# Kernel optimization log

Hardware: AMD Instinct MI355X
Metric: run time of the kernel (lower is better)

Reference implementation:

```python
import jax, jax.numpy as jnp
import numpy as np

LN_EPS = 1e-5  # torch LayerNorm default


def setup_inputs() -> dict:
    key = jax.random.key(0)
    ks = jax.random.split(key, 6)
    N, E, D = 50000, 800000, 128
    x = jax.random.normal(ks[0], (N, D), dtype=jnp.float32)
    edge_index = jax.random.randint(ks[1], (2, E), 0, N, dtype=jnp.int64)
    # Linear params (torch default-ish init scale)
    W = jax.random.normal(ks[2], (D, D), dtype=jnp.float32) / np.sqrt(D)
    b = jax.random.normal(ks[3], (D,), dtype=jnp.float32) * 0.01
    # LayerNorm params
    gamma = jnp.ones((D,), dtype=jnp.float32)
    beta = jnp.zeros((D,), dtype=jnp.float32)
    return {"x": x, "edge_index": edge_index, "W": W, "b": b,
            "gamma": gamma, "beta": beta}


def reference(x, edge_index, W, b, gamma, beta):
    N = x.shape[0]
    # add_self_loops
    loops = jnp.arange(N, dtype=edge_index.dtype)
    row = jnp.concatenate([edge_index[0], loops])  # sources (x_j)
    col = jnp.concatenate([edge_index[1], loops])  # targets (aggregate here)

    h = x @ W.T + b  # [N, D]

    # symmetric normalization: deg computed on row, includes self loops (deg>=1)
    deg = jax.ops.segment_sum(jnp.ones(row.shape, dtype=h.dtype), row,
                              num_segments=N)
    dis = deg ** -0.5
    norm = dis[row] * dis[col]  # [E+N]

    # gather-scale-scatter message passing (aggr='add')
    msg = norm[:, None] * h[row]              # [E+N, D]
    agg = jax.ops.segment_sum(msg, col, num_segments=N)  # [N, D]

    out = jax.nn.relu(agg)
    # dropout: identity (eval mode)
    mu = jnp.mean(out, axis=-1, keepdims=True)
    var = jnp.var(out, axis=-1, keepdims=True)
    out = (out - mu) * jax.lax.rsqrt(var + LN_EPS) * gamma + beta
    return out + x  # residual (in_channels == out_channels, no proj)
```

## Files before the change

### kernel.cpp

```cpp
#include <hip/hip_runtime.h>


#define D 128
#define CHSH 15
#define CHUNK (1 << CHSH)
#define NWORD 12500

typedef short bf16x8 __attribute__((ext_vector_type(8)));
typedef float f32x4 __attribute__((ext_vector_type(4)));

__device__ __forceinline__ unsigned short f2bf(float f) {
    unsigned u = __float_as_uint(f);
    return (unsigned short)((u + 0x7fffu + ((u >> 16) & 1u)) >> 16);
}
__device__ __forceinline__ float bf2f_lo(unsigned v) { return __uint_as_float(v << 16); }
__device__ __forceinline__ float bf2f_hi(unsigned v) { return __uint_as_float(v & 0xffff0000u); }

__global__ void k_cast4(const float4* __restrict__ src, ushort4* __restrict__ dst, int n4) {
    int i = blockIdx.x * 256 + threadIdx.x;
    if (i < n4) {
        float4 v = src[i];
        ushort4 o;
        o.x = f2bf(v.x); o.y = f2bf(v.y); o.z = f2bf(v.z); o.w = f2bf(v.w);
        dst[i] = o;
    }
}

__global__ void __launch_bounds__(1024)
k_gemm_hist(const float* __restrict__ x, const unsigned short* __restrict__ wb,
            const float* __restrict__ bias, unsigned short* __restrict__ hb,
            int nrows,
            const int* __restrict__ ei, int E, int n,
            unsigned char* __restrict__ degc, unsigned char* __restrict__ cntc,
            unsigned char* __restrict__ aux, int K) {
    __shared__ unsigned hist[NWORD];
    int bid = blockIdx.x;
    if (bid < 2 * K) {
        bool is_cnt = bid < K;
        int c = is_cnt ? bid : bid - K;
        const int* vs = is_cnt ? (ei + E) : ei;
        for (int i = threadIdx.x; i < NWORD; i += 1024) hist[i] = 0u;
        __syncthreads();
        int e0 = c << CHSH;
        int e1 = e0 + CHUNK; if (e1 > E) e1 = E;
        if (is_cnt) {
            for (int e = e0 + threadIdx.x; e < e1; e += 1024) {
                int v = vs[e];
                unsigned sh = (v & 3) * 8;
                unsigned old = atomicAdd(&hist[v >> 2], 1u << sh);
                aux[e] = (unsigned char)(old >> sh);
            }
        } else {
            for (int e = e0 + threadIdx.x; e < e1; e += 1024) {
                int v = vs[e];
                atomicAdd(&hist[v >> 2], 1u << ((v & 3) * 8));
            }
        }
        __syncthreads();
        unsigned* dst = (unsigned*)((is_cnt ? cntc : degc) + (size_t)c * n);
        for (int i = threadIdx.x; i < NWORD; i += 1024) dst[i] = hist[i];
    } else {
        int wid = threadIdx.x >> 6, lane = threadIdx.x & 63;
        int m0 = (bid - 2 * K) * 256 + wid * 16;
        if (m0 >= nrows) return;
        int lo16 = lane & 15, quad = lane >> 4;
        const float* arow = x + (size_t)(m0 + lo16) * D + quad * 8;
        bf16x8 a[4];
        #pragma unroll
        for (int kt = 0; kt < 4; kt++) {
            float4 p = *(const float4*)(arow + kt * 32);
            float4 q = *(const float4*)(arow + kt * 32 + 4);
            bf16x8 av;
            av[0] = (short)f2bf(p.x); av[1] = (short)f2bf(p.y);
            av[2] = (short)f2bf(p.z); av[3] = (short)f2bf(p.w);
            av[4] = (short)f2bf(q.x); av[5] = (short)f2bf(q.y);
            av[6] = (short)f2bf(q.z); av[7] = (short)f2bf(q.w);
            a[kt] = av;
        }
        #pragma unroll
        for (int nt = 0; nt < 8; nt++) {
            int n0 = nt * 16;
            const unsigned short* brow = wb + (size_t)(n0 + lo16) * D + quad * 8;
            float bj = bias[n0 + lo16];
            f32x4 acc = {bj, bj, bj, bj};
            #pragma unroll
            for (int kt = 0; kt < 4; kt++) {
                bf16x8 b = *(const bf16x8*)(brow + kt * 32);
                acc = __builtin_amdgcn_mfma_f32_16x16x32_bf16(a[kt], b, acc, 0, 0, 0);
            }
            #pragma unroll
            for (int r = 0; r < 4; r++) {
                int gr = m0 + quad * 4 + r;
                hb[(size_t)gr * D + n0 + lo16] = f2bf(acc[r]);
            }
        }
    }
}

__global__ void k_partial(const unsigned char* __restrict__ degc,
                          const unsigned char* __restrict__ cntc,
                          float* __restrict__ dis, unsigned* __restrict__ cnt,
                          unsigned* __restrict__ partial, int n, int K) {
    __shared__ unsigned s[256];
    int t = threadIdx.x;
    int i = blockIdx.x * 256 + t;
    unsigned tot = 0;
    if (i < n) {
        unsigned d = 0;
        for (int c = 0; c < K; c++) d += degc[(size_t)c * n + i];
        dis[i] = rsqrtf((float)d + 1.0f);
        for (int c = 0; c < K; c++) tot += cntc[(size_t)c * n + i];
        cnt[i] = tot;
    }
    s[t] = tot;
    __syncthreads();
    #pragma unroll
    for (int d = 128; d > 0; d >>= 1) {
        if (t < d) s[t] += s[t + d];
        __syncthreads();
    }
    if (t == 0) partial[blockIdx.x] = s[0];
}

__global__ void k_scanp(unsigned* __restrict__ partial, int nb) {
    __shared__ unsigned s[256];
    int t = threadIdx.x;
    unsigned v = (t < nb) ? partial[t] : 0u;
    s[t] = v;
    __syncthreads();
    #pragma unroll
    for (int d = 1; d < 256; d <<= 1) {
        unsigned u = (t >= d) ? s[t - d] : 0u;
        __syncthreads();
        s[t] += u;
        __syncthreads();
    }
    if (t < nb) partial[t] = s[t] - v;
}

__global__ void k_rowptrc(const unsigned* __restrict__ cnt, const unsigned char* __restrict__ cntc,
                          const unsigned* __restrict__ partial, int n, int E,
                          int* __restrict__ rowptr, int* __restrict__ rowptrc, int K) {
    __shared__ unsigned s[256];
    int t = threadIdx.x;
    int i = blockIdx.x * 256 + t;
    unsigned v = (i < n) ? cnt[i] : 0u;
    s[t] = v;
    __syncthreads();
    #pragma unroll
    for (int d = 1; d < 256; d <<= 1) {
        unsigned u = (t >= d) ? s[t - d] : 0u;
        __syncthreads();
        s[t] += u;
        __syncthreads();
    }
    if (i < n) {
        int base = (int)(partial[blockIdx.x] + s[t] - v);
        rowptr[i] = base;
        unsigned run = 0;
        for (int c = 0; c < K; c++) {
            rowptrc[(size_t)c * n + i] = base + (int)run;
            run += cntc[(size_t)c * n + i];
        }
    }
    if (blockIdx.x == 0 && t == 0) rowptr[n] = E;
}

__global__ void k_fill(const int* __restrict__ ei, int E, int n,
                       const int* __restrict__ rowptrc, const unsigned char* __restrict__ aux,
                       int* __restrict__ srcs) {
    int e = blockIdx.x * 256 + threadIdx.x;
    if (e < E) {
        int r = ei[e];
        int v = ei[E + e];
        int c = e >> CHSH;
        srcs[rowptrc[(size_t)c * n + v] + (int)aux[e]] = r;
    }
}

__global__ void k_agg(const float* __restrict__ x, const unsigned short* __restrict__ hb,
                      const float* __restrict__ dis,
                      const int* __restrict__ rowptr, const int* __restrict__ srcs,
                      const float* __restrict__ gamma, const float* __restrict__ beta,
                      float* __restrict__ out, int n) {
    int wid = threadIdx.x >> 6, lane = threadIdx.x & 63;
    int row = blockIdx.x * 4 + wid;
    if (row >= n) return;
    int q = lane >> 4, t = lane & 15;
    float dc = dis[row];
    float acc[8];
    #pragma unroll
    for (int i = 0; i < 8; i++) acc[i] = 0.0f;
    if (q == 0) {
        uint4 u = ((const uint4*)(hb + (size_t)row * D))[t];
        float sn = dc * dc;
        acc[0] = sn * bf2f_lo(u.x); acc[1] = sn * bf2f_hi(u.x);
        acc[2] = sn * bf2f_lo(u.y); acc[3] = sn * bf2f_hi(u.y);
        acc[4] = sn * bf2f_lo(u.z); acc[5] = sn * bf2f_hi(u.z);
        acc[6] = sn * bf2f_lo(u.w); acc[7] = sn * bf2f_hi(u.w);
    }
    int s0 = rowptr[row];
    int len = rowptr[row + 1] - s0;
    for (int base = 0; base < len; base += 64) {
        int idx = base + lane;
        int sv = (idx < len) ? srcs[s0 + idx] : 0;
        float dv = (idx < len) ? dis[sv] : 0.0f;
        int m = len - base; if (m > 64) m = 64;
        int kmax = (m + 3) >> 2;
        int j = q;
        int r = __shfl(sv, j, 64);
        float nm = dc * __shfl(dv, j, 64);
        uint4 u = ((const uint4*)(hb + (size_t)r * D))[t];
        for (int k = 1; k < kmax; k++) {
            int jn = j + 4;
            int rn = __shfl(sv, jn, 64);
            float nmn = dc * __shfl(dv, jn, 64);
            uint4 un = ((const uint4*)(hb + (size_t)rn * D))[t];
            acc[0] += nm * bf2f_lo(u.x); acc[1] += nm * bf2f_hi(u.x);
            acc[2] += nm * bf2f_lo(u.y); acc[3] += nm * bf2f_hi(u.y);
            acc[4] += nm * bf2f_lo(u.z); acc[5] += nm * bf2f_hi(u.z);
            acc[6] += nm * bf2f_lo(u.w); acc[7] += nm * bf2f_hi(u.w);
            u = un; nm = nmn; j = jn;
        }
        acc[0] += nm * bf2f_lo(u.x); acc[1] += nm * bf2f_hi(u.x);
        acc[2] += nm * bf2f_lo(u.y); acc[3] += nm * bf2f_hi(u.y);
        acc[4] += nm * bf2f_lo(u.z); acc[5] += nm * bf2f_hi(u.z);
        acc[6] += nm * bf2f_lo(u.w); acc[7] += nm * bf2f_hi(u.w);
    }
    #pragma unroll
    for (int i = 0; i < 8; i++) {
        acc[i] += __shfl_xor(acc[i], 16, 64);
        acc[i] += __shfl_xor(acc[i], 32, 64);
        acc[i] = acc[i] > 0.0f ? acc[i] : 0.0f;
    }
    float s1r = 0.0f, s2r = 0.0f;
    #pragma unroll
    for (int i = 0; i < 8; i++) { s1r += acc[i]; s2r += acc[i] * acc[i]; }
    #pragma unroll
    for (int mm = 8; mm >= 1; mm >>= 1) {
        s1r += __shfl_xor(s1r, mm, 64);
        s2r += __shfl_xor(s2r, mm, 64);
    }
    float mean = s1r * (1.0f / 128.0f);
    float var  = s2r * (1.0f / 128.0f) - mean * mean;
    float rstd = rsqrtf(var + 1e-5f);
    if (q == 0) {
        const float4* gr = (const float4*)gamma;
        const float4* br = (const float4*)beta;
        const float4* xr = (const float4*)(x + (size_t)row * D);
        float4* orow = (float4*)(out + (size_t)row * D);
        #pragma unroll
        for (int hf = 0; hf < 2; hf++) {
            float4 g = gr[2 * t + hf], b = br[2 * t + hf], xx = xr[2 * t + hf];
            float4 o;
            o.x = (acc[4 * hf + 0] - mean) * rstd * g.x + b.x + xx.x;
            o.y = (acc[4 * hf + 1] - mean) * rstd * g.y + b.y + xx.y;
            o.z = (acc[4 * hf + 2] - mean) * rstd * g.z + b.z + xx.z;
            o.w = (acc[4 * hf + 3] - mean) * rstd * g.w + b.w + xx.w;
            orow[2 * t + hf] = o;
        }
    }
}

extern "C" void kernel_launch(void* const* d_in, const int* in_sizes, int n_in,
                              void* d_out, int out_size, void* d_ws, size_t ws_size,
                              hipStream_t stream) {
    const float* x     = (const float*)d_in[0];
    const int*   ei    = (const int*)d_in[1];
    const float* W     = (const float*)d_in[2];
    const float* bias  = (const float*)d_in[3];
    const float* gamma = (const float*)d_in[4];
    const float* beta  = (const float*)d_in[5];
    int N = in_sizes[0] / D;
    int E = in_sizes[1] / 2;
    int nb  = (N + 255) / 256;
    int nbE = (E + 255) / 256;
    int K   = (E + CHUNK - 1) >> CHSH;
    int gemm_blocks = (N + 255) / 256;

    char* ws = (char*)d_ws;
    size_t off = 0;
    unsigned short* hb  = (unsigned short*)(ws + off); off += (size_t)N * D * 2;
    unsigned short* wbf = (unsigned short*)(ws + off); off += (size_t)D * D * 2;
    unsigned char* degc = (unsigned char*)(ws + off);  off += (size_t)K * N;
    unsigned char* cntc = (unsigned char*)(ws + off);  off += (size_t)K * N;
    float*    dis       = (float*)(ws + off);          off += (size_t)N * 4;
    unsigned* cnt       = (unsigned*)(ws + off);       off += (size_t)N * 4;
    int*      rowptr    = (int*)(ws + off);            off += (size_t)(N + 1) * 4;
    int*      rowptrc   = (int*)(ws + off);            off += (size_t)K * N * 4;
    unsigned* partial   = (unsigned*)(ws + off);       off += 256 * 4;
    unsigned char* aux  = (unsigned char*)(ws + off);  off += (size_t)E;
    int*      srcs      = (int*)(ws + off);            off += (size_t)E * 4;
    float*    out       = (float*)d_out;

    k_cast4<<<(D * D / 4 + 255) / 256, 256, 0, stream>>>((const float4*)W, (ushort4*)wbf, D * D / 4);
    k_gemm_hist<<<2 * K + gemm_blocks, 1024, 0, stream>>>(x, wbf, bias, hb, N,
                                                          ei, E, N, degc, cntc, aux, K);
    k_partial<<<nb, 256, 0, stream>>>(degc, cntc, dis, cnt, partial, N, K);
    k_scanp<<<1, 256, 0, stream>>>(partial, nb);
    k_rowptrc<<<nb, 256, 0, stream>>>(cnt, cntc, partial, N, E, rowptr, rowptrc, K);
    k_fill<<<nbE, 256, 0, stream>>>(ei, E, N, rowptrc, aux, srcs);
    k_agg<<<(N + 3) / 4, 256, 0, stream>>>(x, hb, dis, rowptr, srcs, gamma, beta, out, N);
}
```

Measured before the change: 179.7 us.

## Fold W cast into GEMM via LDS, merge partial scan, add nontemporal loads

Drops the separate weight-cast kernel. Each GEMM block now converts W to bf16 itself and stores it in shared memory, pre-swizzled into MFMA fragment order. The single-block partial-sum scan kernel is removed: every rowptr block rescans the partials redundantly. Nontemporal loads and stores are added to the streaming accesses in the histogram, fill and aggregation kernels. The aim is to cut two launches and some cache pollution, at the cost of each GEMM block re-reading and converting W before it can start.

```diff
diff --git a/kernel.cpp b/kernel.cpp
--- a/kernel.cpp
+++ b/kernel.cpp
@@ -16,26 +16,17 @@
 __device__ __forceinline__ float bf2f_lo(unsigned v) { return __uint_as_float(v << 16); }
 __device__ __forceinline__ float bf2f_hi(unsigned v) { return __uint_as_float(v & 0xffff0000u); }
 
-__global__ void k_cast4(const float4* __restrict__ src, ushort4* __restrict__ dst, int n4) {
-    int i = blockIdx.x * 256 + threadIdx.x;
-    if (i < n4) {
-        float4 v = src[i];
-        ushort4 o;
-        o.x = f2bf(v.x); o.y = f2bf(v.y); o.z = f2bf(v.z); o.w = f2bf(v.w);
-        dst[i] = o;
-    }
-}
-
 __global__ void __launch_bounds__(1024)
-k_gemm_hist(const float* __restrict__ x, const unsigned short* __restrict__ wb,
+k_gemm_hist(const float* __restrict__ x, const float* __restrict__ W,
             const float* __restrict__ bias, unsigned short* __restrict__ hb,
             int nrows,
             const int* __restrict__ ei, int E, int n,
             unsigned char* __restrict__ degc, unsigned char* __restrict__ cntc,
             unsigned char* __restrict__ aux, int K) {
-    __shared__ unsigned hist[NWORD];
+    __shared__ unsigned sm[NWORD];
     int bid = blockIdx.x;
     if (bid < 2 * K) {
+        unsigned* hist = sm;
         bool is_cnt = bid < K;
         int c = is_cnt ? bid : bid - K;
         const int* vs = is_cnt ? (ei + E) : ei;
@@ -60,6 +51,18 @@
         unsigned* dst = (unsigned*)((is_cnt ? cntc : degc) + (size_t)c * n);
         for (int i = threadIdx.x; i < NWORD; i += 1024) dst[i] = hist[i];
     } else {
+        unsigned short* wf = (unsigned short*)sm;
+        for (int s = threadIdx.x; s < D * D; s += 1024) {
+            int j  = s & 7;
+            int ln = (s >> 3) & 63;
+            int g  = s >> 9;
+            int kt = g & 3, nt = g >> 2;
+            int rw = nt * 16 + (ln & 15);
+            int cl = kt * 32 + (ln >> 4) * 8 + j;
+            wf[s] = f2bf(W[rw * D + cl]);
+        }
+        __syncthreads();
+
         int wid = threadIdx.x >> 6, lane = threadIdx.x & 63;
         int m0 = (bid - 2 * K) * 256 + wid * 16;
         if (m0 >= nrows) return;
@@ -77,15 +80,15 @@
             av[6] = (short)f2bf(q.z); av[7] = (short)f2bf(q.w);
             a[kt] = av;
         }
+        const bf16x8* wfv = (const bf16x8*)wf;
         #pragma unroll
         for (int nt = 0; nt < 8; nt++) {
             int n0 = nt * 16;
-            const unsigned short* brow = wb + (size_t)(n0 + lo16) * D + quad * 8;
             float bj = bias[n0 + lo16];
             f32x4 acc = {bj, bj, bj, bj};
             #pragma unroll
             for (int kt = 0; kt < 4; kt++) {
-                bf16x8 b = *(const bf16x8*)(brow + kt * 32);
+                bf16x8 b = wfv[(nt * 4 + kt) * 64 + lane];
                 acc = __builtin_amdgcn_mfma_f32_16x16x32_bf16(a[kt], b, acc, 0, 0, 0);
             }
             #pragma unroll
@@ -107,7 +110,8 @@
     unsigned tot = 0;
     if (i < n) {
         unsigned d = 0;
-        for (int c = 0; c < K; c++) d += degc[(size_t)c * n + i];
+        for (int c = 0; c < K; c++)
+            d += __builtin_nontemporal_load(degc + (size_t)c * n + i);
         dis[i] = rsqrtf((float)d + 1.0f);
         for (int c = 0; c < K; c++) tot += cntc[(size_t)c * n + i];
         cnt[i] = tot;
@@ -122,40 +126,38 @@
     if (t == 0) partial[blockIdx.x] = s[0];
 }
 
-__global__ void k_scanp(unsigned* __restrict__ partial, int nb) {
-    __shared__ unsigned s[256];
-    int t = threadIdx.x;
-    unsigned v = (t < nb) ? partial[t] : 0u;
-    s[t] = v;
-    __syncthreads();
-    #pragma unroll
-    for (int d = 1; d < 256; d <<= 1) {
-        unsigned u = (t >= d) ? s[t - d] : 0u;
-        __syncthreads();
-        s[t] += u;
-        __syncthreads();
-    }
-    if (t < nb) partial[t] = s[t] - v;
-}
-
 __global__ void k_rowptrc(const unsigned* __restrict__ cnt, const unsigned char* __restrict__ cntc,
                           const unsigned* __restrict__ partial, int n, int E,
-                          int* __restrict__ rowptr, int* __restrict__ rowptrc, int K) {
-    __shared__ unsigned s[256];
+                          int* __restrict__ rowptr, int* __restrict__ rowptrc, int K, int nb) {
+    __shared__ unsigned ps[256];
+    __shared__ unsigned base_sh;
     int t = threadIdx.x;
+    unsigned pv = (t < nb) ? partial[t] : 0u;
+    ps[t] = pv;
+    __syncthreads();
+    #pragma unroll
+    for (int d = 1; d < 256; d <<= 1) {
+        unsigned u = (t >= d) ? ps[t - d] : 0u;
+        __syncthreads();
+        ps[t] += u;
+        __syncthreads();
+    }
+    if (t == blockIdx.x) base_sh = ps[t] - pv;
+    __syncthreads();
+    unsigned bbase = base_sh;
     int i = blockIdx.x * 256 + t;
     unsigned v = (i < n) ? cnt[i] : 0u;
-    s[t] = v;
+    ps[t] = v;
     __syncthreads();
     #pragma unroll
     for (int d = 1; d < 256; d <<= 1) {
-        unsigned u = (t >= d) ? s[t - d] : 0u;
-        __syncthreads();
-        s[t] += u;
+        unsigned u = (t >= d) ? ps[t - d] : 0u;
+        __syncthreads();
+        ps[t] += u;
         __syncthreads();
     }
     if (i < n) {
-        int base = (int)(partial[blockIdx.x] + s[t] - v);
+        int base = (int)(bbase + ps[t] - v);
         rowptr[i] = base;
         unsigned run = 0;
         for (int c = 0; c < K; c++) {
@@ -171,10 +173,11 @@
                        int* __restrict__ srcs) {
     int e = blockIdx.x * 256 + threadIdx.x;
     if (e < E) {
-        int r = ei[e];
-        int v = ei[E + e];
+        int r = __builtin_nontemporal_load(ei + e);
+        int v = __builtin_nontemporal_load(ei + E + e);
         int c = e >> CHSH;
-        srcs[rowptrc[(size_t)c * n + v] + (int)aux[e]] = r;
+        int rank = __builtin_nontemporal_load(aux + e);
+        srcs[rowptrc[(size_t)c * n + v] + rank] = r;
     }
 }
 
@@ -203,7 +206,7 @@
     int len = rowptr[row + 1] - s0;
     for (int base = 0; base < len; base += 64) {
         int idx = base + lane;
-        int sv = (idx < len) ? srcs[s0 + idx] : 0;
+        int sv = (idx < len) ? __builtin_nontemporal_load(srcs + s0 + idx) : 0;
         float dv = (idx < len) ? dis[sv] : 0.0f;
         int m = len - base; if (m > 64) m = 64;
         int kmax = (m + 3) >> 2;
@@ -245,19 +248,20 @@
     float var  = s2r * (1.0f / 128.0f) - mean * mean;
     float rstd = rsqrtf(var + 1e-5f);
     if (q == 0) {
-        const float4* gr = (const float4*)gamma;
-        const float4* br = (const float4*)beta;
-        const float4* xr = (const float4*)(x + (size_t)row * D);
-        float4* orow = (float4*)(out + (size_t)row * D);
+        const f32x4* gr = (const f32x4*)gamma;
+        const f32x4* br = (const f32x4*)beta;
+        const f32x4* xr = (const f32x4*)(x + (size_t)row * D);
+        f32x4* orow = (f32x4*)(out + (size_t)row * D);
         #pragma unroll
         for (int hf = 0; hf < 2; hf++) {
-            float4 g = gr[2 * t + hf], b = br[2 * t + hf], xx = xr[2 * t + hf];
-            float4 o;
-            o.x = (acc[4 * hf + 0] - mean) * rstd * g.x + b.x + xx.x;
-            o.y = (acc[4 * hf + 1] - mean) * rstd * g.y + b.y + xx.y;
-            o.z = (acc[4 * hf + 2] - mean) * rstd * g.z + b.z + xx.z;
-            o.w = (acc[4 * hf + 3] - mean) * rstd * g.w + b.w + xx.w;
-            orow[2 * t + hf] = o;
+            f32x4 g = gr[2 * t + hf], b = br[2 * t + hf];
+            f32x4 xx = __builtin_nontemporal_load(xr + 2 * t + hf);
+            f32x4 o;
+            o[0] = (acc[4 * hf + 0] - mean) * rstd * g[0] + b[0] + xx[0];
+            o[1] = (acc[4 * hf + 1] - mean) * rstd * g[1] + b[1] + xx[1];
+            o[2] = (acc[4 * hf + 2] - mean) * rstd * g[2] + b[2] + xx[2];
+            o[3] = (acc[4 * hf + 3] - mean) * rstd * g[3] + b[3] + xx[3];
+            __builtin_nontemporal_store(o, orow + 2 * t + hf);
         }
     }
 }
@@ -281,7 +285,6 @@
     char* ws = (char*)d_ws;
     size_t off = 0;
     unsigned short* hb  = (unsigned short*)(ws + off); off += (size_t)N * D * 2;
-    unsigned short* wbf = (unsigned short*)(ws + off); off += (size_t)D * D * 2;
     unsigned char* degc = (unsigned char*)(ws + off);  off += (size_t)K * N;
     unsigned char* cntc = (unsigned char*)(ws + off);  off += (size_t)K * N;
     float*    dis       = (float*)(ws + off);          off += (size_t)N * 4;
@@ -293,12 +296,10 @@
     int*      srcs      = (int*)(ws + off);            off += (size_t)E * 4;
     float*    out       = (float*)d_out;
 
-    k_cast4<<<(D * D / 4 + 255) / 256, 256, 0, stream>>>((const float4*)W, (ushort4*)wbf, D * D / 4);
-    k_gemm_hist<<<2 * K + gemm_blocks, 1024, 0, stream>>>(x, wbf, bias, hb, N,
+    k_gemm_hist<<<2 * K + gemm_blocks, 1024, 0, stream>>>(x, W, bias, hb, N,
                                                           ei, E, N, degc, cntc, aux, K);
     k_partial<<<nb, 256, 0, stream>>>(degc, cntc, dis, cnt, partial, N, K);
-    k_scanp<<<1, 256, 0, stream>>>(partial, nb);
-    k_rowptrc<<<nb, 256, 0, stream>>>(cnt, cntc, partial, N, E, rowptr, rowptrc, K);
+    k_rowptrc<<<nb, 256, 0, stream>>>(cnt, cntc, partial, N, E, rowptr, rowptrc, K, nb);
     k_fill<<<nbE, 256, 0, stream>>>(ei, E, N, rowptrc, aux, srcs);
     k_agg<<<(N + 3) / 4, 256, 0, stream>>>(x, hb, dis, rowptr, srcs, gamma, beta, out, N);
 }
```

Result: no change. 181.2 us (+0.9%).
